# Performance work log

Measured on AMD Instinct MI355X. Metric: run time of the kernel, lower is better.

Reference implementation:

```python
import jax, jax.numpy as jnp
import numpy as np

B, T, C, H = 4, 2048, 1024, 16
HD = C // H


def setup_inputs() -> dict:
    key = jax.random.key(0)
    k1, k2, k3, k4 = jax.random.split(key, 4)
    x = jax.random.normal(k1, (B, T, C), dtype=jnp.float32)
    pad_mask = jnp.ones((B, T), dtype=jnp.int32)
    # Linear weights stored as (in, out); torch Linear uses W.T so math is identical.
    w_attn = jax.random.normal(k2, (C, 3 * C), dtype=jnp.float32) * (1.0 / np.sqrt(C))
    w_proj = jax.random.normal(k3, (C, C), dtype=jnp.float32) * (1.0 / np.sqrt(C))
    b_proj = jax.random.normal(k4, (C,), dtype=jnp.float32) * 0.01
    return {"x": x, "pad_mask": pad_mask, "w_attn": w_attn, "w_proj": w_proj, "b_proj": b_proj}


def reference(x, pad_mask, w_attn, w_proj, b_proj):
    Bx, Tx, Cx = x.shape
    hd = Cx // H
    qkv = x @ w_attn                                  # (B,T,3C)
    q, k, v = jnp.split(qkv, 3, axis=2)
    # (B,T,C) -> (B,H,T,hd)
    q = q.reshape(Bx, Tx, H, hd).transpose(0, 2, 1, 3)
    k = k.reshape(Bx, Tx, H, hd).transpose(0, 2, 1, 3)
    v = v.reshape(Bx, Tx, H, hd).transpose(0, 2, 1, 3)
    att = jnp.einsum('bhqd,bhkd->bhqk', q, k) * (1.0 / np.sqrt(hd))
    causal = jnp.tril(jnp.ones((Tx, Tx), dtype=bool))[None, None]       # (1,1,T,T)
    keep = causal & (pad_mask[:, None, None, :] != 0)                   # (B,1,T,T) broadcast
    att = jnp.where(keep, att, -jnp.inf)
    att = jax.nn.softmax(att, axis=-1)
    # dropout p=0.0 (eval) -> identity
    y = jnp.einsum('bhqk,bhkd->bhqd', att, v)
    y = y.transpose(0, 2, 1, 3).reshape(Bx, Tx, Cx)
    return y @ w_proj + b_proj
```

## Files before the change

### kernel.cpp

```cpp
#include <hip/hip_runtime.h>
#include <hip/hip_bf16.h>


using short8  = __attribute__((ext_vector_type(8))) short;
using float4_ = __attribute__((ext_vector_type(4))) float;

#define Bb   4
#define Tt   2048
#define Cc   1024
#define Hh   16
#define HDd  64

__device__ __forceinline__ float bf2f(unsigned short u) {
    union { float f; unsigned int i; } x; x.i = ((unsigned int)u) << 16; return x.f;
}
__device__ __forceinline__ unsigned short f2bf(float f) {
    union { float f; unsigned int i; } x; x.f = f;
    unsigned int r = x.i + 0x7fff + ((x.i >> 16) & 1);
    return (unsigned short)(r >> 16);
}
__device__ __forceinline__ float4_ bmfma(short8 a, short8 b, float4_ c) {
    return __builtin_amdgcn_mfma_f32_16x16x32_bf16(a, b, c, 0, 0, 0);
}
__device__ __forceinline__ float ex2(float x) {
    return __builtin_amdgcn_exp2f(x);
}
__device__ __forceinline__ void gl2lds16(const unsigned short* g, unsigned short* l) {
    __builtin_amdgcn_global_load_lds(
        (const __attribute__((address_space(1))) void*)g,
        (__attribute__((address_space(3))) void*)l, 16, 0, 0);
}

__global__ __launch_bounds__(256) void convert_f32_bf16(
    const float* __restrict__ in, unsigned short* __restrict__ out)
{
    size_t idx = ((size_t)blockIdx.x * 256 + threadIdx.x) * 8;
    float4_ f0 = *(const float4_*)&in[idx];
    float4_ f1 = *(const float4_*)&in[idx + 4];
    short8 h;
    h[0] = (short)f2bf(f0[0]); h[1] = (short)f2bf(f0[1]);
    h[2] = (short)f2bf(f0[2]); h[3] = (short)f2bf(f0[3]);
    h[4] = (short)f2bf(f1[0]); h[5] = (short)f2bf(f1[1]);
    h[6] = (short)f2bf(f1[2]); h[7] = (short)f2bf(f1[3]);
    *(short8*)&out[idx] = h;
}

__global__ __launch_bounds__(256) void transpose_f32_bf16(
    const float* __restrict__ in, unsigned short* __restrict__ out,
    int R, int Ccols)
{
    __shared__ unsigned short tile[32][33];
    int c0 = blockIdx.x * 32, r0 = blockIdx.y * 32;
    int tx = threadIdx.x & 31, ty = threadIdx.x >> 5;
    for (int o = 0; o < 32; o += 8)
        tile[ty + o][tx] = f2bf(in[(size_t)(r0 + ty + o) * Ccols + c0 + tx]);
    __syncthreads();
    for (int o = 0; o < 32; o += 8)
        out[(size_t)(c0 + ty + o) * R + r0 + tx] = tile[tx][ty + o];
}

#define GBK 64

__device__ __forceinline__ void gemm128_main(
    const unsigned short* __restrict__ A, const unsigned short* __restrict__ Bt,
    int K, int m0, int n0,
    unsigned short* As, unsigned short* Bs, float4_ acc[4][4], bool swapT)
{
    int tid  = threadIdx.x;
    int wave = tid >> 6, lane = tid & 63;
    int wm = (wave >> 1) * 64, wn = (wave & 1) * 64;
    int lr = lane & 15, lg = lane >> 4;
    int srow = tid >> 3;
    int scol = (tid & 7) * 8;

    for (int k0 = 0; k0 < K; k0 += GBK) {
        #pragma unroll
        for (int j = 0; j < 4; j++) {
            int row = j * 32 + srow;
            gl2lds16(&A [(size_t)(m0 + row) * K + k0 + scol], &As[row * GBK + scol]);
            gl2lds16(&Bt[(size_t)(n0 + row) * K + k0 + scol], &Bs[row * GBK + scol]);
        }
        __syncthreads();
        #pragma unroll
        for (int ks = 0; ks < GBK; ks += 32) {
            short8 af[4], bf[4];
            #pragma unroll
            for (int i = 0; i < 4; i++) {
                af[i] = *(const short8*)&As[(wm + i * 16 + lr) * GBK + ks + lg * 8];
                bf[i] = *(const short8*)&Bs[(wn + i * 16 + lr) * GBK + ks + lg * 8];
            }
            if (!swapT) {
                #pragma unroll
                for (int i = 0; i < 4; i++)
                    #pragma unroll
                    for (int j = 0; j < 4; j++)
                        acc[i][j] = bmfma(af[i], bf[j], acc[i][j]);
            } else {
                #pragma unroll
                for (int i = 0; i < 4; i++)
                    #pragma unroll
                    for (int j = 0; j < 4; j++)
                        acc[i][j] = bmfma(bf[i], af[j], acc[i][j]);
            }
        }
        __syncthreads();
    }
}

__global__ __launch_bounds__(256) void gemm_qkv(
    const unsigned short* __restrict__ A,
    const unsigned short* __restrict__ Bt,
    unsigned short* __restrict__ Q,
    unsigned short* __restrict__ Ko,
    unsigned short* __restrict__ V)
{
    __shared__ unsigned short As[128 * GBK];
    __shared__ unsigned short Bs[128 * GBK];
    int m0 = blockIdx.x * 128, n0 = blockIdx.y * 128;
    bool vblk = (n0 >= 2048);
    float4_ acc[4][4] = {};
    gemm128_main(A, Bt, 1024, m0, n0, As, Bs, acc, vblk);

    int lane = threadIdx.x & 63, wave = threadIdx.x >> 6;
    int wm = (wave >> 1) * 64, wn = (wave & 1) * 64;
    int lr = lane & 15, lg = lane >> 4;
    if (!vblk) {
        #pragma unroll
        for (int i = 0; i < 4; i++)
            #pragma unroll
            for (int j = 0; j < 4; j++) {
                int n = n0 + wn + 16 * j + lr;
                int which = n >> 10;
                int c = n & 1023;
                int h = c >> 6, d = c & 63;
                unsigned short* dst = (which == 0) ? Q : Ko;
                float sc2 = (which == 0) ? 0.1803368801f : 1.0f;
                #pragma unroll
                for (int r = 0; r < 4; r++) {
                    int m = m0 + wm + 16 * i + lg * 4 + r;
                    int b = m >> 11, t = m & 2047;
                    dst[(((size_t)(b * Hh + h) * Tt) + t) * HDd + d] = f2bf(acc[i][j][r] * sc2);
                }
            }
    } else {
        #pragma unroll
        for (int i = 0; i < 4; i++)
            #pragma unroll
            for (int j = 0; j < 4; j++) {
                int m = m0 + wm + 16 * j + lr;
                int b = m >> 11, t = m & 2047;
                #pragma unroll
                for (int r = 0; r < 4; r++) {
                    int n = n0 + wn + 16 * i + lg * 4 + r;
                    int c = n - 2048;
                    int h = c >> 6, d = c & 63;
                    V[(((size_t)(b * Hh + h) * HDd) + d) * Tt + t] = f2bf(acc[i][j][r]);
                }
            }
    }
}

__global__ __launch_bounds__(256) void gemm_proj(
    const unsigned short* __restrict__ A,
    const unsigned short* __restrict__ Bt,
    const float* __restrict__ bias,
    float* __restrict__ Out)
{
    __shared__ unsigned short As[128 * GBK];
    __shared__ unsigned short Bs[128 * GBK];
    int m0 = blockIdx.x * 128, n0 = blockIdx.y * 128;
    float4_ acc[4][4] = {};
    gemm128_main(A, Bt, 1024, m0, n0, As, Bs, acc, false);

    int lane = threadIdx.x & 63, wave = threadIdx.x >> 6;
    int wm = (wave >> 1) * 64, wn = (wave & 1) * 64;
    int lr = lane & 15, lg = lane >> 4;
    #pragma unroll
    for (int i = 0; i < 4; i++)
        #pragma unroll
        for (int j = 0; j < 4; j++) {
            int n = n0 + wn + 16 * j + lr;
            float bv = bias[n];
            #pragma unroll
            for (int r = 0; r < 4; r++) {
                int m = m0 + wm + 16 * i + lg * 4 + r;
                Out[(size_t)m * 1024 + n] = acc[i][j][r] + bv;
            }
        }
}

#define DPAD 72

__global__ __launch_bounds__(256) void attn_fwd(
    const unsigned short* __restrict__ Q,
    const unsigned short* __restrict__ Kg,
    const unsigned short* __restrict__ Vg,
    const int* __restrict__ pad,
    unsigned short* __restrict__ Y)
{
    __shared__ unsigned short smem[128 * DPAD];
    unsigned short* Kt = smem;
    unsigned short* Vt = smem + 64 * DPAD;

    int flat = blockIdx.x;
    int qb = 31 - (flat >> 6);
    int bh = flat & 63;
    int b  = bh >> 4, h = bh & 15;
    const size_t base = (size_t)bh * Tt * HDd;
    int tid  = threadIdx.x;
    int wave = tid >> 6, lane = tid & 63;
    int lr = lane & 15, lg = lane >> 4;
    int q0 = qb * 64 + wave * 16;
    unsigned short* Pw = &Kt[wave * 16 * DPAD];
    const int* padRow = pad + b * Tt;

    int r8 = tid >> 3;
    int c8 = (tid & 7) * 8;

    short8 qf0 = *(const short8*)&Q[base + (size_t)(q0 + lr) * HDd + lg * 8];
    short8 qf1 = *(const short8*)&Q[base + (size_t)(q0 + lr) * HDd + 32 + lg * 8];

    float m_i[4], l_i[4];
    float4_ o_acc[4];
    #pragma unroll
    for (int r = 0; r < 4; r++) { m_i[r] = -1e30f; l_i[r] = 0.f; }
    #pragma unroll
    for (int dt = 0; dt < 4; dt++) o_acc[dt] = (float4_){0.f, 0.f, 0.f, 0.f};

    for (int kt = 0; kt <= qb; kt++) {
        int k0 = kt * 64;
        {
            short8 ka = *(const short8*)&Kg[base + (size_t)(k0 + r8) * HDd + c8];
            short8 kb = *(const short8*)&Kg[base + (size_t)(k0 + r8 + 32) * HDd + c8];
            short8 va = *(const short8*)&Vg[base + (size_t)r8 * Tt + k0 + c8];
            short8 vb = *(const short8*)&Vg[base + (size_t)(r8 + 32) * Tt + k0 + c8];
            *(short8*)&Kt[r8 * DPAD + c8]        = ka;
            *(short8*)&Kt[(r8 + 32) * DPAD + c8] = kb;
            *(short8*)&Vt[r8 * DPAD + c8]        = va;
            *(short8*)&Vt[(r8 + 32) * DPAD + c8] = vb;
        }
        int pvld = padRow[k0 + lane];
        unsigned long long pm = __ballot(pvld != 0);
        __syncthreads();

        float4_ s[4];
        #pragma unroll
        for (int nt = 0; nt < 4; nt++) {
            short8 kf0 = *(const short8*)&Kt[(nt * 16 + lr) * DPAD + lg * 8];
            short8 kf1 = *(const short8*)&Kt[(nt * 16 + lr) * DPAD + 32 + lg * 8];
            float4_ a = (float4_){0.f, 0.f, 0.f, 0.f};
            a = bmfma(qf0, kf0, a);
            a = bmfma(qf1, kf1, a);
            s[nt] = a;
        }
        if (kt == qb) {
            #pragma unroll
            for (int nt = 0; nt < 4; nt++) {
                int key = k0 + nt * 16 + lr;
                bool kpv = (pm >> (nt * 16 + lr)) & 1ull;
                #pragma unroll
                for (int r = 0; r < 4; r++) {
                    int qrow = q0 + lg * 4 + r;
                    if (!kpv || key > qrow) s[nt][r] = -1e30f;
                }
            }
        } else if (pm != ~0ull) {
            #pragma unroll
            for (int nt = 0; nt < 4; nt++) {
                bool kpv = (pm >> (nt * 16 + lr)) & 1ull;
                #pragma unroll
                for (int r = 0; r < 4; r++)
                    s[nt][r] = kpv ? s[nt][r] : -1e30f;
            }
        }
        float mn[4], alpha[4];
        #pragma unroll
        for (int r = 0; r < 4; r++) {
            float v = fmaxf(fmaxf(s[0][r], s[1][r]), fmaxf(s[2][r], s[3][r]));
            #pragma unroll
            for (int off = 1; off < 16; off <<= 1)
                v = fmaxf(v, __shfl_xor(v, off, 64));
            float m_new = fmaxf(m_i[r], v);
            alpha[r] = ex2(m_i[r] - m_new);
            mn[r] = m_new;
        }
        float rsum[4] = {0.f, 0.f, 0.f, 0.f};
        #pragma unroll
        for (int nt = 0; nt < 4; nt++)
            #pragma unroll
            for (int r = 0; r < 4; r++) {
                float p = ex2(s[nt][r] - mn[r]);
                s[nt][r] = p;
                rsum[r] += p;
            }
        #pragma unroll
        for (int r = 0; r < 4; r++) {
            float v = rsum[r];
            #pragma unroll
            for (int off = 1; off < 16; off <<= 1)
                v += __shfl_xor(v, off, 64);
            l_i[r] = l_i[r] * alpha[r] + v;
            m_i[r] = mn[r];
        }

        __syncthreads();

        #pragma unroll
        for (int nt = 0; nt < 4; nt++)
            #pragma unroll
            for (int r = 0; r < 4; r++)
                Pw[(lg * 4 + r) * DPAD + nt * 16 + lr] = f2bf(s[nt][r]);
        #pragma unroll
        for (int dt = 0; dt < 4; dt++)
            #pragma unroll
            for (int r = 0; r < 4; r++)
                o_acc[dt][r] *= alpha[r];
        short8 pf0 = *(const short8*)&Pw[lr * DPAD + lg * 8];
        short8 pf1 = *(const short8*)&Pw[lr * DPAD + 32 + lg * 8];
        #pragma unroll
        for (int dt = 0; dt < 4; dt++) {
            int d = dt * 16 + lr;
            short8 vf0 = *(const short8*)&Vt[d * DPAD + lg * 8];
            short8 vf1 = *(const short8*)&Vt[d * DPAD + 32 + lg * 8];
            o_acc[dt] = bmfma(pf0, vf0, o_acc[dt]);
            o_acc[dt] = bmfma(pf1, vf1, o_acc[dt]);
        }
        __syncthreads();
    }

    #pragma unroll
    for (int dt = 0; dt < 4; dt++)
        #pragma unroll
        for (int r = 0; r < 4; r++) {
            int qrow = q0 + lg * 4 + r;
            Y[((size_t)b * Tt + qrow) * Cc + h * HDd + dt * 16 + lr] =
                f2bf(o_acc[dt][r] / l_i[r]);
        }
}

extern "C" void kernel_launch(void* const* d_in, const int* in_sizes, int n_in,
                              void* d_out, int out_size, void* d_ws, size_t ws_size,
                              hipStream_t stream)
{
    const float* x      = (const float*)d_in[0];
    const int*   pad    = (const int*)d_in[1];
    const float* w_attn = (const float*)d_in[2];
    const float* w_proj = (const float*)d_in[3];
    const float* b_proj = (const float*)d_in[4];
    float*       out    = (float*)d_out;

    unsigned short* Wta = (unsigned short*)d_ws;
    unsigned short* Wtp = Wta + (size_t)3072 * 1024;
    unsigned short* Xb  = Wtp + (size_t)1024 * 1024;
    unsigned short* Yb  = Xb;
    unsigned short* Qb  = Xb + (size_t)8192 * 1024;
    unsigned short* Kb  = Qb + (size_t)Bb * Hh * Tt * HDd;
    unsigned short* Vb  = Kb + (size_t)Bb * Hh * Tt * HDd;

    convert_f32_bf16<<<dim3(4096), 256, 0, stream>>>(x, Xb);
    transpose_f32_bf16<<<dim3(3072 / 32, 1024 / 32), 256, 0, stream>>>(w_attn, Wta, 1024, 3072);
    transpose_f32_bf16<<<dim3(1024 / 32, 1024 / 32), 256, 0, stream>>>(w_proj, Wtp, 1024, 1024);
    gemm_qkv<<<dim3(8192 / 128, 3072 / 128), 256, 0, stream>>>(Xb, Wta, Qb, Kb, Vb);
    attn_fwd<<<dim3(2048), 256, 0, stream>>>(Qb, Kb, Vb, pad, Yb);
    gemm_proj<<<dim3(8192 / 128, 1024 / 128), 256, 0, stream>>>(Yb, Wtp, b_proj, out);
}
```

Measured before the change: 314.2 us.

## Transpose score MFMA in attention, swizzle P stores, supertile GEMM blocks

The attention kernel swaps the MFMA operands so each lane holds one query row's scores. Row max and sum then need two cross-lane shuffles instead of four per row, and the per-row softmax state shrinks to scalars. P is written to LDS as 4-element vectors through an XOR swizzle to reduce bank conflicts, and alpha and l are broadcast back with shuffles. Both GEMMs remap block indices into 8x8 supertiles for better L2 reuse, which adds extra shuffles and more complex indexing.

```diff
diff --git a/kernel.cpp b/kernel.cpp
--- a/kernel.cpp
+++ b/kernel.cpp
@@ -3,6 +3,7 @@
 
 
 using short8  = __attribute__((ext_vector_type(8))) short;
+using short4_ = __attribute__((ext_vector_type(4))) short;
 using float4_ = __attribute__((ext_vector_type(4))) float;
 
 #define Bb   4
@@ -107,6 +108,14 @@
     }
 }
 
+__device__ __forceinline__ void supertile_remap(int& m0, int& n0)
+{
+    int bx = blockIdx.x, by = blockIdx.y;
+    int mt = ((by & 7) << 3) | (bx & 7);
+    int nt = ((by >> 3) << 3) | (bx >> 3);
+    m0 = mt * 128; n0 = nt * 128;
+}
+
 __global__ __launch_bounds__(256) void gemm_qkv(
     const unsigned short* __restrict__ A,
     const unsigned short* __restrict__ Bt,
@@ -116,7 +125,8 @@
 {
     __shared__ unsigned short As[128 * GBK];
     __shared__ unsigned short Bs[128 * GBK];
-    int m0 = blockIdx.x * 128, n0 = blockIdx.y * 128;
+    int m0, n0;
+    supertile_remap(m0, n0);
     bool vblk = (n0 >= 2048);
     float4_ acc[4][4] = {};
     gemm128_main(A, Bt, 1024, m0, n0, As, Bs, acc, vblk);
@@ -168,7 +178,8 @@
 {
     __shared__ unsigned short As[128 * GBK];
     __shared__ unsigned short Bs[128 * GBK];
-    int m0 = blockIdx.x * 128, n0 = blockIdx.y * 128;
+    int m0, n0;
+    supertile_remap(m0, n0);
     float4_ acc[4][4] = {};
     gemm128_main(A, Bt, 1024, m0, n0, As, Bs, acc, false);
 
@@ -220,12 +231,14 @@
     short8 qf0 = *(const short8*)&Q[base + (size_t)(q0 + lr) * HDd + lg * 8];
     short8 qf1 = *(const short8*)&Q[base + (size_t)(q0 + lr) * HDd + 32 + lg * 8];
 
-    float m_i[4], l_i[4];
+    float m_i = -1e30f, l_i = 0.f;
     float4_ o_acc[4];
     #pragma unroll
-    for (int r = 0; r < 4; r++) { m_i[r] = -1e30f; l_i[r] = 0.f; }
-    #pragma unroll
     for (int dt = 0; dt < 4; dt++) o_acc[dt] = (float4_){0.f, 0.f, 0.f, 0.f};
+
+    int c7 = lr & 7;
+    int ebase = (lg & 1) * 4;
+    int hnib = lg >> 1;
 
     for (int kt = 0; kt <= qb; kt++) {
         int k0 = kt * 64;
@@ -249,74 +262,71 @@
             short8 kf0 = *(const short8*)&Kt[(nt * 16 + lr) * DPAD + lg * 8];
             short8 kf1 = *(const short8*)&Kt[(nt * 16 + lr) * DPAD + 32 + lg * 8];
             float4_ a = (float4_){0.f, 0.f, 0.f, 0.f};
-            a = bmfma(qf0, kf0, a);
-            a = bmfma(qf1, kf1, a);
+            a = bmfma(kf0, qf0, a);
+            a = bmfma(kf1, qf1, a);
             s[nt] = a;
         }
         if (kt == qb) {
             #pragma unroll
-            for (int nt = 0; nt < 4; nt++) {
-                int key = k0 + nt * 16 + lr;
-                bool kpv = (pm >> (nt * 16 + lr)) & 1ull;
+            for (int nt = 0; nt < 4; nt++)
                 #pragma unroll
                 for (int r = 0; r < 4; r++) {
-                    int qrow = q0 + lg * 4 + r;
-                    if (!kpv || key > qrow) s[nt][r] = -1e30f;
+                    int kl = nt * 16 + lg * 4 + r;
+                    bool kpv = (pm >> kl) & 1ull;
+                    if (!kpv || kl > wave * 16 + lr) s[nt][r] = -1e30f;
                 }
-            }
         } else if (pm != ~0ull) {
             #pragma unroll
-            for (int nt = 0; nt < 4; nt++) {
-                bool kpv = (pm >> (nt * 16 + lr)) & 1ull;
-                #pragma unroll
-                for (int r = 0; r < 4; r++)
+            for (int nt = 0; nt < 4; nt++)
+                #pragma unroll
+                for (int r = 0; r < 4; r++) {
+                    int kl = nt * 16 + lg * 4 + r;
+                    bool kpv = (pm >> kl) & 1ull;
                     s[nt][r] = kpv ? s[nt][r] : -1e30f;
-            }
-        }
-        float mn[4], alpha[4];
+                }
+        }
+        float v = fmaxf(fmaxf(s[0][0], s[0][1]), fmaxf(s[0][2], s[0][3]));
+        #pragma unroll
+        for (int nt = 1; nt < 4; nt++)
+            v = fmaxf(v, fmaxf(fmaxf(s[nt][0], s[nt][1]), fmaxf(s[nt][2], s[nt][3])));
+        v = fmaxf(v, __shfl_xor(v, 16, 64));
+        v = fmaxf(v, __shfl_xor(v, 32, 64));
+        float m_new = fmaxf(m_i, v);
+        float alpha = ex2(m_i - m_new);
+        float rsum = 0.f;
+        #pragma unroll
+        for (int nt = 0; nt < 4; nt++)
+            #pragma unroll
+            for (int r = 0; r < 4; r++) {
+                float p = ex2(s[nt][r] - m_new);
+                s[nt][r] = p;
+                rsum += p;
+            }
+        rsum += __shfl_xor(rsum, 16, 64);
+        rsum += __shfl_xor(rsum, 32, 64);
+        l_i = l_i * alpha + rsum;
+        m_i = m_new;
+
         #pragma unroll
         for (int r = 0; r < 4; r++) {
-            float v = fmaxf(fmaxf(s[0][r], s[1][r]), fmaxf(s[2][r], s[3][r]));
-            #pragma unroll
-            for (int off = 1; off < 16; off <<= 1)
-                v = fmaxf(v, __shfl_xor(v, off, 64));
-            float m_new = fmaxf(m_i[r], v);
-            alpha[r] = ex2(m_i[r] - m_new);
-            mn[r] = m_new;
-        }
-        float rsum[4] = {0.f, 0.f, 0.f, 0.f};
-        #pragma unroll
-        for (int nt = 0; nt < 4; nt++)
-            #pragma unroll
-            for (int r = 0; r < 4; r++) {
-                float p = ex2(s[nt][r] - mn[r]);
-                s[nt][r] = p;
-                rsum[r] += p;
-            }
-        #pragma unroll
-        for (int r = 0; r < 4; r++) {
-            float v = rsum[r];
-            #pragma unroll
-            for (int off = 1; off < 16; off <<= 1)
-                v += __shfl_xor(v, off, 64);
-            l_i[r] = l_i[r] * alpha[r] + v;
-            m_i[r] = mn[r];
-        }
-
-        __syncthreads();
-
-        #pragma unroll
-        for (int nt = 0; nt < 4; nt++)
-            #pragma unroll
-            for (int r = 0; r < 4; r++)
-                Pw[(lg * 4 + r) * DPAD + nt * 16 + lr] = f2bf(s[nt][r]);
-        #pragma unroll
-        for (int dt = 0; dt < 4; dt++)
-            #pragma unroll
-            for (int r = 0; r < 4; r++)
-                o_acc[dt][r] *= alpha[r];
-        short8 pf0 = *(const short8*)&Pw[lr * DPAD + lg * 8];
-        short8 pf1 = *(const short8*)&Pw[lr * DPAD + 32 + lg * 8];
+            float ar = __shfl(alpha, (lg << 2) + r, 64);
+            #pragma unroll
+            for (int dt = 0; dt < 4; dt++)
+                o_acc[dt][r] *= ar;
+        }
+
+        __syncthreads();
+
+        #pragma unroll
+        for (int nt = 0; nt < 4; nt++) {
+            short4_ w;
+            w[0] = (short)f2bf(s[nt][0]); w[1] = (short)f2bf(s[nt][1]);
+            w[2] = (short)f2bf(s[nt][2]); w[3] = (short)f2bf(s[nt][3]);
+            int blk = ((2 * nt + hnib) ^ c7);
+            *(short4_*)&Pw[lr * DPAD + blk * 8 + ebase] = w;
+        }
+        short8 pf0 = *(const short8*)&Pw[lr * DPAD + ((lg ^ c7) << 3)];
+        short8 pf1 = *(const short8*)&Pw[lr * DPAD + (((4 + lg) ^ c7) << 3)];
         #pragma unroll
         for (int dt = 0; dt < 4; dt++) {
             int d = dt * 16 + lr;
@@ -329,13 +339,14 @@
     }
 
     #pragma unroll
-    for (int dt = 0; dt < 4; dt++)
-        #pragma unroll
-        for (int r = 0; r < 4; r++) {
-            int qrow = q0 + lg * 4 + r;
+    for (int r = 0; r < 4; r++) {
+        float lr_ = __shfl(l_i, (lg << 2) + r, 64);
+        int qrow = q0 + lg * 4 + r;
+        #pragma unroll
+        for (int dt = 0; dt < 4; dt++)
             Y[((size_t)b * Tt + qrow) * Cc + h * HDd + dt * 16 + lr] =
-                f2bf(o_acc[dt][r] / l_i[r]);
-        }
+                f2bf(o_acc[dt][r] / lr_);
+    }
 }
 
 extern "C" void kernel_launch(void* const* d_in, const int* in_sizes, int n_in,
```

Measured after the change: 306.2 us. 1.03x faster.
